# Performance work log

Measured on AMD Instinct MI355X. Metric: run time of the kernel, lower is better.

Reference implementation:

```python
import jax, jax.numpy as jnp
import numpy as np

K = 76          # model dim = 6 + 30 + 30 + 10 (concat of modality embeddings)
H = 8           # heads; per-head dim == K (wide attention variant)
D = 6           # depth
T = 1024        # seq_length (frames)
B = 8           # batch
C = 2           # num_classes
EPS = 1e-5


def setup_inputs() -> dict:
    key = jax.random.key(0)
    ks = jax.random.split(key, 24)
    rn = lambda k, shape, s=0.02: (jax.random.normal(k, shape, jnp.float32) * s)
    return {
        # forward inputs (per-frame multimodal features)
        "v": jax.random.normal(ks[0], (B, T, 6), jnp.float32),
        "x": jax.random.normal(ks[1], (B, T, 137), jnp.float32),
        "y": jax.random.normal(ks[2], (B, T, 113), jnp.float32),
        "z": jax.random.normal(ks[3], (B, T, 35), jnp.float32),
        # modality embed linears (stored (in, out); torch does x @ W.T)
        "W_hp": rn(ks[4], (6, 6)),     "b_hp": jnp.zeros((6,), jnp.float32),
        "W_lm": rn(ks[5], (137, 30)),  "b_lm": jnp.zeros((30,), jnp.float32),
        "W_el": rn(ks[6], (113, 30)),  "b_el": jnp.zeros((30,), jnp.float32),
        "W_au": rn(ks[7], (35, 10)),   "b_au": jnp.zeros((10,), jnp.float32),
        "pos_emb": rn(ks[8], (T, K)),
        # per-block params stacked over depth for lax.scan
        "Wq": rn(ks[9], (D, K, H * K)),
        "Wk": rn(ks[10], (D, K, H * K)),
        "Wv": rn(ks[11], (D, K, H * K)),
        "Wu": rn(ks[12], (D, H * K, K)), "bu": jnp.zeros((D, K), jnp.float32),
        "ln1_s": jnp.ones((D, K), jnp.float32), "ln1_b": jnp.zeros((D, K), jnp.float32),
        "W1": rn(ks[13], (D, K, 4 * K)), "b1": jnp.zeros((D, 4 * K), jnp.float32),
        "W2": rn(ks[14], (D, 4 * K, K)), "b2": jnp.zeros((D, K), jnp.float32),
        "ln2_s": jnp.ones((D, K), jnp.float32), "ln2_b": jnp.zeros((D, K), jnp.float32),
        "W_out": rn(ks[15], (K, C)), "b_out": jnp.zeros((C,), jnp.float32),
    }


def _layernorm(h, s, b):
    mu = jnp.mean(h, axis=-1, keepdims=True)
    var = jnp.mean(jnp.square(h - mu), axis=-1, keepdims=True)
    return (h - mu) * jax.lax.rsqrt(var + EPS) * s + b


def reference(v, x, y, z,
              W_hp, b_hp, W_lm, b_lm, W_el, b_el, W_au, b_au,
              pos_emb, Wq, Wk, Wv, Wu, bu, ln1_s, ln1_b,
              W1, b1, W2, b2, ln2_s, ln2_b, W_out, b_out):
    b, t = v.shape[0], v.shape[1]
    tokens = jnp.concatenate([
        v @ W_hp + b_hp,
        x @ W_lm + b_lm,
        y @ W_el + b_el,
        z @ W_au + b_au,
    ], axis=2)                                   # (b, t, K)
    h = tokens + pos_emb[None, :, :]
    scale = 1.0 / np.sqrt(K)                     # dot / sqrt(e), e == k

    def block(hh, p):
        wq, wk, wv, wu, bu_, l1s, l1b, w1, b1_, w2, b2_, l2s, l2b = p
        # (b, t, H*K) -> (b, H, t, K); per-head dim is full K here
        q = (hh @ wq).reshape(b, t, H, K).transpose(0, 2, 1, 3)
        k_ = (hh @ wk).reshape(b, t, H, K).transpose(0, 2, 1, 3)
        vv = (hh @ wv).reshape(b, t, H, K).transpose(0, 2, 1, 3)
        dot = jax.nn.softmax(jnp.einsum('bhte,bhse->bhts', q, k_) * scale, axis=-1)
        att = jnp.einsum('bhts,bhse->bhte', dot, vv)        # (b, H, t, K)
        att = att.transpose(0, 2, 1, 3).reshape(b, t, H * K)
        att = att @ wu + bu_                                # unify heads -> (b, t, K)
        h1 = _layernorm(att + hh, l1s, l1b)
        ff = jax.nn.relu(h1 @ w1 + b1_) @ w2 + b2_
        return _layernorm(ff + h1, l2s, l2b), None

    h, _ = jax.lax.scan(
        block, h,
        (Wq, Wk, Wv, Wu, bu, ln1_s, ln1_b, W1, b1, W2, b2, ln2_s, ln2_b))
    return h @ W_out + b_out                     # (b, t, num_classes)
```

## Files before the change

kernel.cpp:

```cpp
#include <hip/hip_runtime.h>
#include <hip/hip_bf16.h>
#include <math.h>

#define B_   8
#define T_   1024
#define K_   76
#define KP_  96
#define H_   8
#define D_   6
#define C_   2
#define HK_  608
#define QKLD_ 640
#define FF_  304
#define FFP_ 320
#define EK_  320
#define BT_  8192
#define EPS_ 1e-5f
#define SCL2_ (0.11470786693528088f * 1.4426950408889634f)

typedef unsigned short u16;
typedef unsigned int u32;
typedef short bf16x8 __attribute__((ext_vector_type(8)));
typedef float f32x4 __attribute__((ext_vector_type(4)));

__device__ __forceinline__ u16 f2b(float f) {
  __hip_bfloat16 h = __float2bfloat16(f);
  return *reinterpret_cast<u16*>(&h);
}
__device__ __forceinline__ float b2f(u16 u) {
  __hip_bfloat16 h = *reinterpret_cast<__hip_bfloat16*>(&u);
  return __bfloat162float(h);
}
__device__ __forceinline__ u32 pack2(float a, float b) {
  __hip_bfloat162 t = __float22bfloat162_rn(make_float2(a, b));
  return *reinterpret_cast<u32*>(&t);
}

#define PER_L_ 304128ULL
__global__ __launch_bounds__(256) void wconv_kernel(
    const float* __restrict__ Wq, const float* __restrict__ Wk, const float* __restrict__ Wv,
    const float* __restrict__ Wu, const float* __restrict__ W1, const float* __restrict__ W2,
    u16* __restrict__ WT) {
  __shared__ float Ls[32][65];
  int zz = blockIdx.y;
  int d = zz / 6, wt = zz % 6;
  const float* in; int Kd, Nsrc, Nalloc, Kp; u16* out;
  size_t lb = (size_t)d * PER_L_;
  switch (wt) {
    case 0: in = Wq + (size_t)d*K_*HK_; Kd=K_;  Nsrc=HK_; Nalloc=640; Kp=KP_;  out = WT + lb;          break;
    case 1: in = Wk + (size_t)d*K_*HK_; Kd=K_;  Nsrc=HK_; Nalloc=640; Kp=KP_;  out = WT + lb + 61440;  break;
    case 2: in = Wv + (size_t)d*K_*HK_; Kd=K_;  Nsrc=HK_; Nalloc=640; Kp=KP_;  out = WT + lb + 122880; break;
    case 3: in = Wu + (size_t)d*HK_*K_; Kd=HK_; Nsrc=K_;  Nalloc=96;  Kp=HK_;  out = WT + lb + 184320; break;
    case 4: in = W1 + (size_t)d*K_*FF_; Kd=K_;  Nsrc=FF_; Nalloc=320; Kp=KP_;  out = WT + lb + 242688; break;
    default:in = W2 + (size_t)d*FF_*K_; Kd=FF_; Nsrc=K_;  Nalloc=96;  Kp=FFP_; out = WT + lb + 273408; break;
  }
  int tiles_k = Kp / 32;
  int tiles_n = (Nalloc + 63) / 64;
  int tile = blockIdx.x;
  if (tile >= tiles_k * tiles_n) return;
  int tn = tile / tiles_k, tk = tile % tiles_k;
  int n0 = tn * 64, k0 = tk * 32;
  for (int i = threadIdx.x; i < 2048; i += 256) {
    int kk = i >> 6, nn = i & 63;
    int gk = k0 + kk, gn = n0 + nn;
    int srccol = gn;
    if (wt < 3) {
      int hh8 = gn / 80, ft = gn - hh8 * 80;
      srccol = (ft < 76) ? (hh8 * 76 + ft) : -1;
    }
    Ls[kk][nn] = (gk < Kd && srccol >= 0 && srccol < Nsrc) ? in[(size_t)gk * Nsrc + srccol] : 0.f;
  }
  __syncthreads();
  for (int i = threadIdx.x; i < 2048; i += 256) {
    int nn = i >> 5, kk = i & 31;
    int gn = n0 + nn;
    if (gn < Nalloc) out[(size_t)gn * Kp + k0 + kk] = f2b(Ls[kk][nn]);
  }
}

__global__ void wembed_kernel(const float* __restrict__ W_hp, const float* __restrict__ b_hp,
                              const float* __restrict__ W_lm, const float* __restrict__ b_lm,
                              const float* __restrict__ W_el, const float* __restrict__ b_el,
                              const float* __restrict__ W_au, const float* __restrict__ b_au,
                              u16* __restrict__ WE) {
  int idx = blockIdx.x * 256 + threadIdx.x;
  if (idx >= 96 * EK_) return;
  int n = idx / EK_, kk = idx % EK_;
  float val = 0.f;
  if (n < 76) {
    if (kk < 6) { if (n < 6) val = W_hp[kk * 6 + n]; }
    else if (kk < 143) { int i = kk - 6; if (n >= 6 && n < 36) val = W_lm[i * 30 + (n - 6)]; }
    else if (kk < 256) { int i = kk - 143; if (n >= 36 && n < 66) val = W_el[i * 30 + (n - 36)]; }
    else if (kk < 291) { int i = kk - 256; if (n >= 66) val = W_au[i * 10 + (n - 66)]; }
    else if (kk == 291) {
      val = (n < 6) ? b_hp[n] : (n < 36) ? b_lm[n - 6] : (n < 66) ? b_el[n - 36] : b_au[n - 66];
    }
  }
  WE[idx] = f2b(val);
}

__global__ void pack_kernel(const float* __restrict__ v, const float* __restrict__ x,
                            const float* __restrict__ y, const float* __restrict__ z,
                            u16* __restrict__ xin) {
  int idx = blockIdx.x * 256 + threadIdx.x;
  if (idx >= BT_ * (EK_ / 2)) return;
  int bt = idx / (EK_ / 2), dc = idx % (EK_ / 2);
  int c0 = dc * 2;
  auto fetch = [&](int c) -> float {
    if (c < 6) return v[bt * 6 + c];
    if (c < 143) return x[bt * 137 + c - 6];
    if (c < 256) return y[bt * 113 + c - 143];
    if (c < 291) return z[bt * 35 + c - 256];
    if (c == 291) return 1.0f;
    return 0.f;
  };
  ((u32*)xin)[idx] = pack2(fetch(c0), fetch(c0 + 1));
}

template<int RT, int CT, int KSTEPS, int RELU, int TPB>
__global__ __launch_bounds__(TPB) void gemm_kernel(
    const u16* __restrict__ A, int lda,
    const u16* __restrict__ Wt, int ldw, unsigned long long wstride,
    const float* __restrict__ bias,
    u16* __restrict__ Cc, int ldc, int N,
    int ksplit, int klen, unsigned long long osplit,
    float cs,
    u16* __restrict__ vbt,
    const float* __restrict__ pos) {
  __shared__ u16 Bs[CT * 16 * 56];
  const int tid = threadIdx.x;
  const int w = tid >> 6, lane = tid & 63;
  const int r = lane & 15, g = lane >> 4;
  const int n0 = blockIdx.x * CT * 16;
  const int m0 = blockIdx.y * (TPB / 64) * 16 * RT;
  const int z = blockIdx.z;
  const int k0 = z * ksplit;
  const int kend = k0 + klen;
  const u16* Wz = Wt + (size_t)z * wstride;
  const float* bias_eff = (z == 0) ? bias : nullptr;
  const float csz = (z == 0) ? cs : 1.f;
  u16* Cz = Cc + (size_t)z * osplit;
  constexpr int NB = (CT * 64 + TPB - 1) / TPB;

  const f32x4 fz = {0.f, 0.f, 0.f, 0.f};
  f32x4 acc[RT][CT];
  #pragma unroll
  for (int rt = 0; rt < RT; rt++)
    #pragma unroll
    for (int ct = 0; ct < CT; ct++) acc[rt][ct] = fz;

  bf16x8 a_all[RT][KSTEPS];
  #pragma unroll
  for (int rt = 0; rt < RT; rt++) {
    const u16* arow = A + (size_t)(m0 + (w * RT + rt) * 16 + r) * lda;
    #pragma unroll
    for (int ks = 0; ks < KSTEPS; ks++) {
      int kA = k0 + ks * 32 + g * 8;
      if (kA < kend) a_all[rt][ks] = *(const bf16x8*)(arow + kA);
      else a_all[rt][ks] = bf16x8{0, 0, 0, 0, 0, 0, 0, 0};
    }
  }

  uint4 bpre[NB];
  auto loadB = [&](int ks) {
    int kk = k0 + ks * 32;
    #pragma unroll
    for (int i0 = 0; i0 < NB; i0++) {
      int idx = tid + i0 * TPB;
      bpre[i0] = make_uint4(0, 0, 0, 0);
      if (idx < CT * 64) {
        int nn = idx >> 2, kc = idx & 3;
        if (kk + kc * 8 < kend)
          bpre[i0] = *(const uint4*)(Wz + (size_t)(n0 + nn) * ldw + kk + kc * 8);
      }
    }
  };
  loadB(0);

  for (int ks = 0; ks < KSTEPS; ks++) {
    __syncthreads();
    #pragma unroll
    for (int i0 = 0; i0 < NB; i0++) {
      int idx = tid + i0 * TPB;
      if (idx < CT * 64) {
        int nn = idx >> 2, kc = idx & 3;
        *(uint4*)&Bs[nn * 56 + (((kc ^ (nn & 3)) << 3))] = bpre[i0];
      }
    }
    __syncthreads();
    if (ks + 1 < KSTEPS) loadB(ks + 1);
    #pragma unroll
    for (int ct = 0; ct < CT; ct++) {
      bf16x8 bb = *(const bf16x8*)&Bs[(ct * 16 + r) * 56 + (((g ^ (r & 3)) << 3))];
      #pragma unroll
      for (int rt = 0; rt < RT; rt++)
        acc[rt][ct] = __builtin_amdgcn_mfma_f32_16x16x32_bf16(a_all[rt][ks], bb, acc[rt][ct], 0, 0, 0);
    }
  }

  if (vbt && z == 2) {
    #pragma unroll
    for (int rt = 0; rt < RT; rt++) {
      #pragma unroll
      for (int ct = 0; ct < CT; ct++) {
        int feat = ct * 16 + r;
        int token = m0 + (w * RT + rt) * 16 + g * 4;
        int bb_ = token >> 10, tt = token & 1023;
        ushort4 pk;
        if (feat < 76) {
          pk.x = f2b(acc[rt][ct][0]); pk.y = f2b(acc[rt][ct][1]);
          pk.z = f2b(acc[rt][ct][2]); pk.w = f2b(acc[rt][ct][3]);
        } else {
          pk = make_ushort4(0, 0, 0, 0);
        }
        *(ushort4*)(vbt + (((size_t)(bb_ * 8 + blockIdx.x) * 80 + feat) << 10) + tt) = pk;
      }
    }
  } else {
    #pragma unroll
    for (int rt = 0; rt < RT; rt++) {
      #pragma unroll
      for (int ct = 0; ct < CT; ct++) {
        int col = n0 + ct * 16 + r;
        if (col < ldc) {
          #pragma unroll
          for (int reg = 0; reg < 4; reg++) {
            int row = m0 + (w * RT + rt) * 16 + g * 4 + reg;
            float val = acc[rt][ct][reg] * csz;
            if (bias_eff && col < N) val += bias_eff[col];
            if (pos && col < N) val += pos[(row & (T_ - 1)) * K_ + col];
            if (RELU) val = fmaxf(val, 0.f);
            Cz[(size_t)row * ldc + col] = f2b(val);
          }
        }
      }
    }
  }
}

__global__ __launch_bounds__(64) void ffn_kernel(
    const u16* __restrict__ att, const u16* __restrict__ WuT, const float* __restrict__ bu,
    const u16* __restrict__ hres, const float* __restrict__ l1s, const float* __restrict__ l1b,
    const u16* __restrict__ W1T, const float* __restrict__ b1,
    const u16* __restrict__ W2T, const float* __restrict__ b2,
    const float* __restrict__ l2s, const float* __restrict__ l2b,
    u16* __restrict__ hout) {
  __shared__ u16 Bs[6 * 16 * 56];
  __shared__ u16 h1s[16 * 104];
  __shared__ u16 ffs[16 * 328];
  const int lane = threadIdx.x & 63;
  const int r = lane & 15, g = lane >> 4;
  const int m0 = blockIdx.x * 16;
  const f32x4 fz = {0.f, 0.f, 0.f, 0.f};

  u16 resv[4][6];
  #pragma unroll
  for (int reg = 0; reg < 4; reg++)
    #pragma unroll
    for (int ct = 0; ct < 6; ct++)
      resv[reg][ct] = hres[(size_t)(m0 + g * 4 + reg) * KP_ + ct * 16 + r];

  bf16x8 a1[19];
  {
    const u16* arow = att + (size_t)(m0 + r) * HK_;
    #pragma unroll
    for (int ks = 0; ks < 19; ks++) a1[ks] = *(const bf16x8*)(arow + ks * 32 + g * 8);
  }
  f32x4 acc1[6];
  #pragma unroll
  for (int ct = 0; ct < 6; ct++) acc1[ct] = fz;
  {
    uint4 bpre[6];
    auto loadB1 = [&](int ks) {
      #pragma unroll
      for (int i0 = 0; i0 < 6; i0++) {
        int idx = lane + i0 * 64;
        int nn = idx >> 2, kc = idx & 3;
        bpre[i0] = *(const uint4*)(WuT + (size_t)nn * HK_ + ks * 32 + kc * 8);
      }
    };
    loadB1(0);
    for (int ks = 0; ks < 19; ks++) {
      #pragma unroll
      for (int i0 = 0; i0 < 6; i0++) {
        int idx = lane + i0 * 64;
        int nn = idx >> 2, kc = idx & 3;
        *(uint4*)&Bs[nn * 56 + ((kc ^ (nn & 3)) << 3)] = bpre[i0];
      }
      if (ks + 1 < 19) loadB1(ks + 1);
      #pragma unroll
      for (int ct = 0; ct < 6; ct++) {
        bf16x8 bb = *(const bf16x8*)&Bs[(ct * 16 + r) * 56 + ((g ^ (r & 3)) << 3)];
        acc1[ct] = __builtin_amdgcn_mfma_f32_16x16x32_bf16(a1[ks], bb, acc1[ct], 0, 0, 0);
      }
    }
  }
  #pragma unroll
  for (int reg = 0; reg < 4; reg++) {
    float vals[6];
    float s = 0.f, s2 = 0.f;
    #pragma unroll
    for (int ct = 0; ct < 6; ct++) {
      int col = ct * 16 + r;
      float val = 0.f;
      if (col < K_) {
        val = acc1[ct][reg] + bu[col] + b2f(resv[reg][ct]);
        s += val; s2 += val * val;
      }
      vals[ct] = val;
    }
    #pragma unroll
    for (int m = 1; m < 16; m <<= 1) { s += __shfl_xor(s, m); s2 += __shfl_xor(s2, m); }
    float mu = s * (1.f / 76.f);
    float rstd = rsqrtf(s2 * (1.f / 76.f) - mu * mu + EPS_);
    #pragma unroll
    for (int ct = 0; ct < 6; ct++) {
      int col = ct * 16 + r;
      u16 ov = 0;
      if (col < K_) ov = f2b((vals[ct] - mu) * rstd * l1s[col] + l1b[col]);
      h1s[(g * 4 + reg) * 104 + col] = ov;
    }
  }

  bf16x8 a2[3];
  #pragma unroll
  for (int ks = 0; ks < 3; ks++)
    a2[ks] = *(const bf16x8*)&h1s[r * 104 + ks * 32 + g * 8];
  f32x4 acc2[20];
  #pragma unroll
  for (int ct = 0; ct < 20; ct++) acc2[ct] = fz;
  #pragma unroll
  for (int ks = 0; ks < 3; ks++) {
    bf16x8 bb[20];
    #pragma unroll
    for (int ct = 0; ct < 20; ct++)
      bb[ct] = *(const bf16x8*)(W1T + (size_t)(ct * 16 + r) * KP_ + ks * 32 + g * 8);
    #pragma unroll
    for (int ct = 0; ct < 20; ct++)
      acc2[ct] = __builtin_amdgcn_mfma_f32_16x16x32_bf16(a2[ks], bb[ct], acc2[ct], 0, 0, 0);
  }
  #pragma unroll
  for (int reg = 0; reg < 4; reg++)
    #pragma unroll
    for (int ct = 0; ct < 20; ct++) {
      int col = ct * 16 + r;
      float val = acc2[ct][reg] + ((col < FF_) ? b1[col] : 0.f);
      ffs[(g * 4 + reg) * 328 + col] = f2b(fmaxf(val, 0.f));
    }

  bf16x8 a3[10];
  #pragma unroll
  for (int ks = 0; ks < 10; ks++)
    a3[ks] = *(const bf16x8*)&ffs[r * 328 + ks * 32 + g * 8];
  f32x4 acc3[6];
  #pragma unroll
  for (int ct = 0; ct < 6; ct++) acc3[ct] = fz;
  {
    uint4 bpre[6];
    auto loadB3 = [&](int ks) {
      #pragma unroll
      for (int i0 = 0; i0 < 6; i0++) {
        int idx = lane + i0 * 64;
        int nn = idx >> 2, kc = idx & 3;
        bpre[i0] = *(const uint4*)(W2T + (size_t)nn * FFP_ + ks * 32 + kc * 8);
      }
    };
    loadB3(0);
    for (int ks = 0; ks < 10; ks++) {
      #pragma unroll
      for (int i0 = 0; i0 < 6; i0++) {
        int idx = lane + i0 * 64;
        int nn = idx >> 2, kc = idx & 3;
        *(uint4*)&Bs[nn * 56 + ((kc ^ (nn & 3)) << 3)] = bpre[i0];
      }
      if (ks + 1 < 10) loadB3(ks + 1);
      #pragma unroll
      for (int ct = 0; ct < 6; ct++) {
        bf16x8 bb = *(const bf16x8*)&Bs[(ct * 16 + r) * 56 + ((g ^ (r & 3)) << 3)];
        acc3[ct] = __builtin_amdgcn_mfma_f32_16x16x32_bf16(a3[ks], bb, acc3[ct], 0, 0, 0);
      }
    }
  }
  #pragma unroll
  for (int reg = 0; reg < 4; reg++) {
    float vals[6];
    float s = 0.f, s2 = 0.f;
    #pragma unroll
    for (int ct = 0; ct < 6; ct++) {
      int col = ct * 16 + r;
      float val = 0.f;
      if (col < K_) {
        val = acc3[ct][reg] + b2[col] + b2f(h1s[(g * 4 + reg) * 104 + col]);
        s += val; s2 += val * val;
      }
      vals[ct] = val;
    }
    #pragma unroll
    for (int m = 1; m < 16; m <<= 1) { s += __shfl_xor(s, m); s2 += __shfl_xor(s2, m); }
    float mu = s * (1.f / 76.f);
    float rstd = rsqrtf(s2 * (1.f / 76.f) - mu * mu + EPS_);
    u16* outr = hout + (size_t)(m0 + g * 4 + reg) * KP_;
    #pragma unroll
    for (int ct = 0; ct < 6; ct++) {
      int col = ct * 16 + r;
      u16 ov = 0;
      if (col < K_) ov = f2b((vals[ct] - mu) * rstd * l2s[col] + l2b[col]);
      outr[col] = ov;
    }
  }
}

__global__ __launch_bounds__(256, 3) void attn_kernel(const u16* __restrict__ q,
                                                      const u16* __restrict__ k,
                                                      const u16* __restrict__ vbt,
                                                      u16* __restrict__ att) {
  __shared__ u16 Ks[64 * 104];
  __shared__ u16 Vs[80 * 72];
  __shared__ u32 Psw[128 * 36];
  const int bid = blockIdx.x;
  const int hh = bid & 7, b = (bid >> 3) & 7, qt = bid >> 6;
  const int tid = threadIdx.x;
  const int w = tid >> 6, lane = tid & 63;
  const int r = lane & 15, g = lane >> 4;
  const int qbase = b * T_ + qt * 128;

  bf16x8 aq[2][3];
  #pragma unroll
  for (int rt = 0; rt < 2; rt++) {
    const u16* qsrc = q + (size_t)(qbase + w * 32 + rt * 16 + r) * QKLD_ + hh * 80;
    #pragma unroll
    for (int ks = 0; ks < 3; ks++) {
      int e0 = ks * 32 + g * 8;
      aq[rt][ks] = (e0 < 80) ? *(const bf16x8*)(qsrc + e0) : bf16x8{0, 0, 0, 0, 0, 0, 0, 0};
    }
  }

  const int krow = tid >> 2, kq4 = tid & 3;
  uint4 kpre[3], vpre[3];
  auto stage_load = [&](int kt) {
    const int kb = b * T_ + kt * 64;
    const u16* ksrc = k + (size_t)(kb + krow) * QKLD_ + hh * 80;
    #pragma unroll
    for (int i = 0; i < 3; i++) {
      int c = kq4 + 4 * i;
      kpre[i] = (c < 10) ? *(const uint4*)(ksrc + c * 8) : make_uint4(0, 0, 0, 0);
    }
    const u16* vsrc = vbt + (((size_t)(b * 8 + hh) * 80) << 10) + kt * 64;
    #pragma unroll
    for (int p = 0; p < 3; p++) {
      int idx = tid + p * 256;
      vpre[p] = (idx < 640) ? *(const uint4*)(vsrc + ((size_t)(idx >> 3) << 10) + (idx & 7) * 8)
                            : make_uint4(0, 0, 0, 0);
    }
  };
  auto stage_write = [&]() {
    #pragma unroll
    for (int i = 0; i < 3; i++) {
      int c = kq4 + 4 * i;
      *(uint4*)&Ks[krow * 104 + c * 8] = kpre[i];
    }
    #pragma unroll
    for (int p = 0; p < 3; p++) {
      int idx = tid + p * 256;
      if (idx < 640)
        *(uint4*)&Vs[(idx >> 3) * 72 + (idx & 7) * 8] = vpre[p];
    }
  };

  u32* Pw = Psw + w * 32 * 36;

  const f32x4 fz = {0.f, 0.f, 0.f, 0.f};
  f32x4 o[2][5];
  float ls[2] = {0.f, 0.f};
  #pragma unroll
  for (int rt = 0; rt < 2; rt++)
    #pragma unroll
    for (int i = 0; i < 5; i++) o[rt][i] = fz;

  stage_load(0);

  for (int kt = 0; kt < 16; kt++) {
    __syncthreads();
    stage_write();
    __syncthreads();
    if (kt < 15) stage_load(kt + 1);

    f32x4 st[2][4];
    #pragma unroll
    for (int ct = 0; ct < 4; ct++) { st[0][ct] = fz; st[1][ct] = fz; }
    __builtin_amdgcn_s_setprio(1);
    #pragma unroll
    for (int ct = 0; ct < 4; ct++) {
      #pragma unroll
      for (int ks = 0; ks < 3; ks++) {
        bf16x8 ak = *(const bf16x8*)&Ks[(ct * 16 + r) * 104 + ks * 32 + g * 8];
        st[0][ct] = __builtin_amdgcn_mfma_f32_16x16x32_bf16(ak, aq[0][ks], st[0][ct], 0, 0, 0);
        st[1][ct] = __builtin_amdgcn_mfma_f32_16x16x32_bf16(ak, aq[1][ks], st[1][ct], 0, 0, 0);
      }
    }
    __builtin_amdgcn_s_setprio(0);

    #pragma unroll
    for (int rt = 0; rt < 2; rt++) {
      float rs = 0.f;
      u32 pk[8];
      #pragma unroll
      for (int ct = 0; ct < 4; ct++) {
        float p0 = exp2f(st[rt][ct][0]), p1 = exp2f(st[rt][ct][1]);
        float p2 = exp2f(st[rt][ct][2]), p3 = exp2f(st[rt][ct][3]);
        rs += (p0 + p1) + (p2 + p3);
        pk[ct * 2] = pack2(p0, p1);
        pk[ct * 2 + 1] = pack2(p2, p3);
      }
      ls[rt] += rs;
      u32* pw = Pw + (rt * 16 + r) * 36;
      #pragma unroll
      for (int ct = 0; ct < 4; ct++)
        *(uint2*)(pw + ct * 8 + g * 2) = make_uint2(pk[ct * 2], pk[ct * 2 + 1]);
    }

    bf16x8 pa[2][2];
    #pragma unroll
    for (int rt = 0; rt < 2; rt++) {
      const u32* pr = Pw + (rt * 16 + r) * 36;
      #pragma unroll
      for (int ks = 0; ks < 2; ks++) {
        uint4 t = *(const uint4*)(pr + ks * 16 + g * 4);
        pa[rt][ks] = *reinterpret_cast<bf16x8*>(&t);
      }
    }
    __builtin_amdgcn_s_setprio(1);
    #pragma unroll
    for (int ks = 0; ks < 2; ks++) {
      #pragma unroll
      for (int c5 = 0; c5 < 5; c5++) {
        bf16x8 av = *(const bf16x8*)&Vs[(c5 * 16 + r) * 72 + ks * 32 + g * 8];
        #pragma unroll
        for (int rt = 0; rt < 2; rt++)
          o[rt][c5] = __builtin_amdgcn_mfma_f32_16x16x32_bf16(av, pa[rt][ks], o[rt][c5], 0, 0, 0);
      }
    }
    __builtin_amdgcn_s_setprio(0);
  }

  #pragma unroll
  for (int rt = 0; rt < 2; rt++) {
    ls[rt] += __shfl_xor(ls[rt], 16);
    ls[rt] += __shfl_xor(ls[rt], 32);
    float inv = 1.f / ls[rt];
    int token = qbase + w * 32 + rt * 16 + r;
    #pragma unroll
    for (int c5 = 0; c5 < 5; c5++) {
      if (c5 == 4 && g == 3) continue;
      ushort4 pk4;
      pk4.x = f2b(o[rt][c5][0] * inv);
      pk4.y = f2b(o[rt][c5][1] * inv);
      pk4.z = f2b(o[rt][c5][2] * inv);
      pk4.w = f2b(o[rt][c5][3] * inv);
      *(ushort4*)&att[(size_t)token * HK_ + hh * 76 + c5 * 16 + g * 4] = pk4;
    }
  }
}

__global__ void out_kernel(const u16* __restrict__ h, const float* __restrict__ W,
                           const float* __restrict__ bias, float* __restrict__ out) {
  int bt = blockIdx.x * 256 + threadIdx.x;
  if (bt >= BT_) return;
  const u32* hr = (const u32*)(h + (size_t)bt * KP_);
  float acc0 = bias[0], acc1 = bias[1];
  #pragma unroll 4
  for (int d = 0; d < 38; d++) {
    u32 h2 = hr[d];
    float f0 = b2f((u16)(h2 & 0xffff)), f1 = b2f((u16)(h2 >> 16));
    acc0 += f0 * W[(2 * d) * 2] + f1 * W[(2 * d + 1) * 2];
    acc1 += f0 * W[(2 * d) * 2 + 1] + f1 * W[(2 * d + 1) * 2 + 1];
  }
  out[bt * 2] = acc0;
  out[bt * 2 + 1] = acc1;
}

extern "C" void kernel_launch(void* const* d_in, const int* in_sizes, int n_in,
                              void* d_out, int out_size, void* d_ws, size_t ws_size,
                              hipStream_t stream) {
  const float* v    = (const float*)d_in[0];
  const float* x    = (const float*)d_in[1];
  const float* y    = (const float*)d_in[2];
  const float* z    = (const float*)d_in[3];
  const float* W_hp = (const float*)d_in[4];
  const float* b_hp = (const float*)d_in[5];
  const float* W_lm = (const float*)d_in[6];
  const float* b_lm = (const float*)d_in[7];
  const float* W_el = (const float*)d_in[8];
  const float* b_el = (const float*)d_in[9];
  const float* W_au = (const float*)d_in[10];
  const float* b_au = (const float*)d_in[11];
  const float* pos  = (const float*)d_in[12];
  const float* Wq   = (const float*)d_in[13];
  const float* Wk   = (const float*)d_in[14];
  const float* Wv   = (const float*)d_in[15];
  const float* Wu   = (const float*)d_in[16];
  const float* bu   = (const float*)d_in[17];
  const float* ln1s = (const float*)d_in[18];
  const float* ln1b = (const float*)d_in[19];
  const float* W1   = (const float*)d_in[20];
  const float* b1   = (const float*)d_in[21];
  const float* W2   = (const float*)d_in[22];
  const float* b2   = (const float*)d_in[23];
  const float* ln2s = (const float*)d_in[24];
  const float* ln2b = (const float*)d_in[25];
  const float* Wout = (const float*)d_in[26];
  const float* bout = (const float*)d_in[27];

  u16* ws  = (u16*)d_ws;
  u16* WT  = ws;
  u16* WE  = WT + 1824768;
  u16* h   = WE + 30720;
  u16* xin = h + 786432;
  u16* qb  = xin + 2621440;
  u16* kb  = qb + 5242880;
  u16* vbt = kb + 5242880;
  u16* att = vbt + 5242880;
  u16* h1  = att + 4980736;

  wconv_kernel<<<dim3(38, 36), 256, 0, stream>>>(Wq, Wk, Wv, Wu, W1, W2, WT);
  wembed_kernel<<<(96 * EK_ + 255) / 256, 256, 0, stream>>>(
      W_hp, b_hp, W_lm, b_lm, W_el, b_el, W_au, b_au, WE);
  pack_kernel<<<(BT_ * (EK_ / 2) + 255) / 256, 256, 0, stream>>>(v, x, y, z, xin);
  gemm_kernel<1, 6, 10, 0, 128><<<dim3(1, 256, 1), 128, 0, stream>>>(
      xin, EK_, WE, EK_, 0ULL, nullptr, h, KP_, K_, 0, EK_, 0ULL,
      1.f, nullptr, pos);

  for (int d = 0; d < D_; d++) {
    u16* WTd = WT + (size_t)d * PER_L_;
    const float* bu_d = bu + (size_t)d * K_;
    const float* l1s  = ln1s + (size_t)d * K_;
    const float* l1b  = ln1b + (size_t)d * K_;
    const float* b1_d = b1 + (size_t)d * FF_;
    const float* b2_d = b2 + (size_t)d * K_;
    const float* l2s  = ln2s + (size_t)d * K_;
    const float* l2b  = ln2b + (size_t)d * K_;

    gemm_kernel<2, 5, 3, 0, 256><<<dim3(8, 64, 3), 256, 0, stream>>>(
        h, KP_, WTd, KP_, 61440ULL, nullptr, qb, QKLD_, QKLD_, 0, KP_, 5242880ULL,
        SCL2_, vbt, nullptr);
    attn_kernel<<<dim3(512), 256, 0, stream>>>(qb, kb, vbt, att);
    ffn_kernel<<<dim3(512), 64, 0, stream>>>(
        att, WTd + 184320, bu_d, h, l1s, l1b,
        WTd + 242688, b1_d, WTd + 273408, b2_d, l2s, l2b, h);
  }

  out_kernel<<<(BT_ + 255) / 256, 256, 0, stream>>>(h, Wout, bout, (float*)d_out);
}
```

Before: 571.3 us.

## Merge prep kernels, fuse output head into FFN, halve attention tile size

Folds the three preprocessing launches into one prep kernel that dispatches on block index. Moves the final output projection into the last layer's FFN epilogue using a shuffle reduction, which removes a separate launch and a reread of h. It also changes attention from 128-query tiles with 256 threads to 64-query tiles with 128 threads over 1024 blocks, using different K/V staging and zeroed pad columns. This trades fewer launches and better occupancy against reloading each K/V tile for twice as many blocks.

```diff
diff --git a/kernel.cpp b/kernel.cpp
--- a/kernel.cpp
+++ b/kernel.cpp
@@ -37,84 +37,84 @@
 }
 
 #define PER_L_ 304128ULL
-__global__ __launch_bounds__(256) void wconv_kernel(
+__global__ __launch_bounds__(256) void prep_kernel(
     const float* __restrict__ Wq, const float* __restrict__ Wk, const float* __restrict__ Wv,
     const float* __restrict__ Wu, const float* __restrict__ W1, const float* __restrict__ W2,
-    u16* __restrict__ WT) {
+    u16* __restrict__ WT,
+    const float* __restrict__ W_hp, const float* __restrict__ b_hp,
+    const float* __restrict__ W_lm, const float* __restrict__ b_lm,
+    const float* __restrict__ W_el, const float* __restrict__ b_el,
+    const float* __restrict__ W_au, const float* __restrict__ b_au,
+    u16* __restrict__ WE,
+    const float* __restrict__ v, const float* __restrict__ x,
+    const float* __restrict__ y, const float* __restrict__ z,
+    u16* __restrict__ xin) {
   __shared__ float Ls[32][65];
-  int zz = blockIdx.y;
-  int d = zz / 6, wt = zz % 6;
-  const float* in; int Kd, Nsrc, Nalloc, Kp; u16* out;
-  size_t lb = (size_t)d * PER_L_;
-  switch (wt) {
-    case 0: in = Wq + (size_t)d*K_*HK_; Kd=K_;  Nsrc=HK_; Nalloc=640; Kp=KP_;  out = WT + lb;          break;
-    case 1: in = Wk + (size_t)d*K_*HK_; Kd=K_;  Nsrc=HK_; Nalloc=640; Kp=KP_;  out = WT + lb + 61440;  break;
-    case 2: in = Wv + (size_t)d*K_*HK_; Kd=K_;  Nsrc=HK_; Nalloc=640; Kp=KP_;  out = WT + lb + 122880; break;
-    case 3: in = Wu + (size_t)d*HK_*K_; Kd=HK_; Nsrc=K_;  Nalloc=96;  Kp=HK_;  out = WT + lb + 184320; break;
-    case 4: in = W1 + (size_t)d*K_*FF_; Kd=K_;  Nsrc=FF_; Nalloc=320; Kp=KP_;  out = WT + lb + 242688; break;
-    default:in = W2 + (size_t)d*FF_*K_; Kd=FF_; Nsrc=K_;  Nalloc=96;  Kp=FFP_; out = WT + lb + 273408; break;
-  }
-  int tiles_k = Kp / 32;
-  int tiles_n = (Nalloc + 63) / 64;
-  int tile = blockIdx.x;
-  if (tile >= tiles_k * tiles_n) return;
-  int tn = tile / tiles_k, tk = tile % tiles_k;
-  int n0 = tn * 64, k0 = tk * 32;
-  for (int i = threadIdx.x; i < 2048; i += 256) {
-    int kk = i >> 6, nn = i & 63;
-    int gk = k0 + kk, gn = n0 + nn;
-    int srccol = gn;
-    if (wt < 3) {
-      int hh8 = gn / 80, ft = gn - hh8 * 80;
-      srccol = (ft < 76) ? (hh8 * 76 + ft) : -1;
-    }
-    Ls[kk][nn] = (gk < Kd && srccol >= 0 && srccol < Nsrc) ? in[(size_t)gk * Nsrc + srccol] : 0.f;
-  }
-  __syncthreads();
-  for (int i = threadIdx.x; i < 2048; i += 256) {
-    int nn = i >> 5, kk = i & 31;
-    int gn = n0 + nn;
-    if (gn < Nalloc) out[(size_t)gn * Kp + k0 + kk] = f2b(Ls[kk][nn]);
-  }
-}
-
-__global__ void wembed_kernel(const float* __restrict__ W_hp, const float* __restrict__ b_hp,
-                              const float* __restrict__ W_lm, const float* __restrict__ b_lm,
-                              const float* __restrict__ W_el, const float* __restrict__ b_el,
-                              const float* __restrict__ W_au, const float* __restrict__ b_au,
-                              u16* __restrict__ WE) {
-  int idx = blockIdx.x * 256 + threadIdx.x;
-  if (idx >= 96 * EK_) return;
-  int n = idx / EK_, kk = idx % EK_;
-  float val = 0.f;
-  if (n < 76) {
-    if (kk < 6) { if (n < 6) val = W_hp[kk * 6 + n]; }
-    else if (kk < 143) { int i = kk - 6; if (n >= 6 && n < 36) val = W_lm[i * 30 + (n - 6)]; }
-    else if (kk < 256) { int i = kk - 143; if (n >= 36 && n < 66) val = W_el[i * 30 + (n - 36)]; }
-    else if (kk < 291) { int i = kk - 256; if (n >= 66) val = W_au[i * 10 + (n - 66)]; }
-    else if (kk == 291) {
-      val = (n < 6) ? b_hp[n] : (n < 36) ? b_lm[n - 6] : (n < 66) ? b_el[n - 36] : b_au[n - 66];
-    }
-  }
-  WE[idx] = f2b(val);
-}
-
-__global__ void pack_kernel(const float* __restrict__ v, const float* __restrict__ x,
-                            const float* __restrict__ y, const float* __restrict__ z,
-                            u16* __restrict__ xin) {
-  int idx = blockIdx.x * 256 + threadIdx.x;
-  if (idx >= BT_ * (EK_ / 2)) return;
-  int bt = idx / (EK_ / 2), dc = idx % (EK_ / 2);
-  int c0 = dc * 2;
-  auto fetch = [&](int c) -> float {
-    if (c < 6) return v[bt * 6 + c];
-    if (c < 143) return x[bt * 137 + c - 6];
-    if (c < 256) return y[bt * 113 + c - 143];
-    if (c < 291) return z[bt * 35 + c - 256];
-    if (c == 291) return 1.0f;
-    return 0.f;
-  };
-  ((u32*)xin)[idx] = pack2(fetch(c0), fetch(c0 + 1));
+  const int bid = blockIdx.x;
+  if (bid < 1368) {
+    int tile = bid % 38, zz = bid / 38;
+    int d = zz / 6, wt = zz % 6;
+    const float* in; int Kd, Nsrc, Nalloc, Kp; u16* out;
+    size_t lb = (size_t)d * PER_L_;
+    switch (wt) {
+      case 0: in = Wq + (size_t)d*K_*HK_; Kd=K_;  Nsrc=HK_; Nalloc=640; Kp=KP_;  out = WT + lb;          break;
+      case 1: in = Wk + (size_t)d*K_*HK_; Kd=K_;  Nsrc=HK_; Nalloc=640; Kp=KP_;  out = WT + lb + 61440;  break;
+      case 2: in = Wv + (size_t)d*K_*HK_; Kd=K_;  Nsrc=HK_; Nalloc=640; Kp=KP_;  out = WT + lb + 122880; break;
+      case 3: in = Wu + (size_t)d*HK_*K_; Kd=HK_; Nsrc=K_;  Nalloc=96;  Kp=HK_;  out = WT + lb + 184320; break;
+      case 4: in = W1 + (size_t)d*K_*FF_; Kd=K_;  Nsrc=FF_; Nalloc=320; Kp=KP_;  out = WT + lb + 242688; break;
+      default:in = W2 + (size_t)d*FF_*K_; Kd=FF_; Nsrc=K_;  Nalloc=96;  Kp=FFP_; out = WT + lb + 273408; break;
+    }
+    int tiles_k = Kp / 32;
+    int tiles_n = (Nalloc + 63) / 64;
+    if (tile >= tiles_k * tiles_n) return;
+    int tn = tile / tiles_k, tk = tile % tiles_k;
+    int n0 = tn * 64, k0 = tk * 32;
+    for (int i = threadIdx.x; i < 2048; i += 256) {
+      int kk = i >> 6, nn = i & 63;
+      int gk = k0 + kk, gn = n0 + nn;
+      int srccol = gn;
+      if (wt < 3) {
+        int hh8 = gn / 80, ft = gn - hh8 * 80;
+        srccol = (ft < 76) ? (hh8 * 76 + ft) : -1;
+      }
+      Ls[kk][nn] = (gk < Kd && srccol >= 0 && srccol < Nsrc) ? in[(size_t)gk * Nsrc + srccol] : 0.f;
+    }
+    __syncthreads();
+    for (int i = threadIdx.x; i < 2048; i += 256) {
+      int nn = i >> 5, kk = i & 31;
+      int gn = n0 + nn;
+      if (gn < Nalloc) out[(size_t)gn * Kp + k0 + kk] = f2b(Ls[kk][nn]);
+    }
+  } else if (bid < 1488) {
+    int idx = (bid - 1368) * 256 + threadIdx.x;
+    if (idx >= 96 * EK_) return;
+    int n = idx / EK_, kk = idx % EK_;
+    float val = 0.f;
+    if (n < 76) {
+      if (kk < 6) { if (n < 6) val = W_hp[kk * 6 + n]; }
+      else if (kk < 143) { int i = kk - 6; if (n >= 6 && n < 36) val = W_lm[i * 30 + (n - 6)]; }
+      else if (kk < 256) { int i = kk - 143; if (n >= 36 && n < 66) val = W_el[i * 30 + (n - 36)]; }
+      else if (kk < 291) { int i = kk - 256; if (n >= 66) val = W_au[i * 10 + (n - 66)]; }
+      else if (kk == 291) {
+        val = (n < 6) ? b_hp[n] : (n < 36) ? b_lm[n - 6] : (n < 66) ? b_el[n - 36] : b_au[n - 66];
+      }
+    }
+    WE[idx] = f2b(val);
+  } else {
+    int idx = (bid - 1488) * 256 + threadIdx.x;
+    if (idx >= BT_ * (EK_ / 2)) return;
+    int bt = idx / (EK_ / 2), dc = idx % (EK_ / 2);
+    int c0 = dc * 2;
+    auto fetch = [&](int c) -> float {
+      if (c < 6) return v[bt * 6 + c];
+      if (c < 143) return x[bt * 137 + c - 6];
+      if (c < 256) return y[bt * 113 + c - 143];
+      if (c < 291) return z[bt * 35 + c - 256];
+      if (c == 291) return 1.0f;
+      return 0.f;
+    };
+    ((u32*)xin)[idx] = pack2(fetch(c0), fetch(c0 + 1));
+  }
 }
 
 template<int RT, int CT, int KSTEPS, int RELU, int TPB>
@@ -244,7 +244,9 @@
     const u16* __restrict__ W1T, const float* __restrict__ b1,
     const u16* __restrict__ W2T, const float* __restrict__ b2,
     const float* __restrict__ l2s, const float* __restrict__ l2b,
-    u16* __restrict__ hout) {
+    u16* __restrict__ hout,
+    const float* __restrict__ Wout, const float* __restrict__ bout,
+    float* __restrict__ outp) {
   __shared__ u16 Bs[6 * 16 * 56];
   __shared__ u16 h1s[16 * 104];
   __shared__ u16 ffs[16 * 328];
@@ -400,29 +402,51 @@
     float mu = s * (1.f / 76.f);
     float rstd = rsqrtf(s2 * (1.f / 76.f) - mu * mu + EPS_);
     u16* outr = hout + (size_t)(m0 + g * 4 + reg) * KP_;
+    float p0 = 0.f, p1 = 0.f;
     #pragma unroll
     for (int ct = 0; ct < 6; ct++) {
       int col = ct * 16 + r;
       u16 ov = 0;
-      if (col < K_) ov = f2b((vals[ct] - mu) * rstd * l2s[col] + l2b[col]);
+      if (col < K_) {
+        float vln = (vals[ct] - mu) * rstd * l2s[col] + l2b[col];
+        ov = f2b(vln);
+        if (outp) {
+          p0 += vln * Wout[col * 2];
+          p1 += vln * Wout[col * 2 + 1];
+        }
+      }
       outr[col] = ov;
     }
-  }
-}
-
-__global__ __launch_bounds__(256, 3) void attn_kernel(const u16* __restrict__ q,
+    if (outp) {
+      #pragma unroll
+      for (int m = 1; m < 16; m <<= 1) { p0 += __shfl_xor(p0, m); p1 += __shfl_xor(p1, m); }
+      if (r == 0) {
+        int row = m0 + g * 4 + reg;
+        outp[row * 2] = p0 + bout[0];
+        outp[row * 2 + 1] = p1 + bout[1];
+      }
+    }
+  }
+}
+
+__global__ __launch_bounds__(128, 2) void attn_kernel(const u16* __restrict__ q,
                                                       const u16* __restrict__ k,
                                                       const u16* __restrict__ vbt,
                                                       u16* __restrict__ att) {
   __shared__ u16 Ks[64 * 104];
   __shared__ u16 Vs[80 * 72];
-  __shared__ u32 Psw[128 * 36];
+  __shared__ u32 Psw[64 * 36];
   const int bid = blockIdx.x;
   const int hh = bid & 7, b = (bid >> 3) & 7, qt = bid >> 6;
   const int tid = threadIdx.x;
   const int w = tid >> 6, lane = tid & 63;
   const int r = lane & 15, g = lane >> 4;
-  const int qbase = b * T_ + qt * 128;
+  const int qbase = b * T_ + qt * 64;
+
+  {
+    int row = tid >> 1, off = 80 + (tid & 1) * 8;
+    *(uint4*)&Ks[row * 104 + off] = make_uint4(0, 0, 0, 0);
+  }
 
   bf16x8 aq[2][3];
   #pragma unroll
@@ -435,35 +459,29 @@
     }
   }
 
-  const int krow = tid >> 2, kq4 = tid & 3;
-  uint4 kpre[3], vpre[3];
+  const int krow = tid >> 1, kq2 = tid & 1;
+  uint4 kpre[5], vpre[5];
   auto stage_load = [&](int kt) {
     const int kb = b * T_ + kt * 64;
     const u16* ksrc = k + (size_t)(kb + krow) * QKLD_ + hh * 80;
     #pragma unroll
-    for (int i = 0; i < 3; i++) {
-      int c = kq4 + 4 * i;
-      kpre[i] = (c < 10) ? *(const uint4*)(ksrc + c * 8) : make_uint4(0, 0, 0, 0);
-    }
+    for (int i = 0; i < 5; i++)
+      kpre[i] = *(const uint4*)(ksrc + (kq2 + 2 * i) * 8);
     const u16* vsrc = vbt + (((size_t)(b * 8 + hh) * 80) << 10) + kt * 64;
     #pragma unroll
-    for (int p = 0; p < 3; p++) {
-      int idx = tid + p * 256;
-      vpre[p] = (idx < 640) ? *(const uint4*)(vsrc + ((size_t)(idx >> 3) << 10) + (idx & 7) * 8)
-                            : make_uint4(0, 0, 0, 0);
+    for (int p = 0; p < 5; p++) {
+      int idx = tid + p * 128;
+      vpre[p] = *(const uint4*)(vsrc + ((size_t)(idx >> 3) << 10) + (idx & 7) * 8);
     }
   };
   auto stage_write = [&]() {
     #pragma unroll
-    for (int i = 0; i < 3; i++) {
-      int c = kq4 + 4 * i;
-      *(uint4*)&Ks[krow * 104 + c * 8] = kpre[i];
-    }
-    #pragma unroll
-    for (int p = 0; p < 3; p++) {
-      int idx = tid + p * 256;
-      if (idx < 640)
-        *(uint4*)&Vs[(idx >> 3) * 72 + (idx & 7) * 8] = vpre[p];
+    for (int i = 0; i < 5; i++)
+      *(uint4*)&Ks[krow * 104 + (kq2 + 2 * i) * 8] = kpre[i];
+    #pragma unroll
+    for (int p = 0; p < 5; p++) {
+      int idx = tid + p * 128;
+      *(uint4*)&Vs[(idx >> 3) * 72 + (idx & 7) * 8] = vpre[p];
     }
   };
 
@@ -560,23 +578,6 @@
       *(ushort4*)&att[(size_t)token * HK_ + hh * 76 + c5 * 16 + g * 4] = pk4;
     }
   }
-}
-
-__global__ void out_kernel(const u16* __restrict__ h, const float* __restrict__ W,
-                           const float* __restrict__ bias, float* __restrict__ out) {
-  int bt = blockIdx.x * 256 + threadIdx.x;
-  if (bt >= BT_) return;
-  const u32* hr = (const u32*)(h + (size_t)bt * KP_);
-  float acc0 = bias[0], acc1 = bias[1];
-  #pragma unroll 4
-  for (int d = 0; d < 38; d++) {
-    u32 h2 = hr[d];
-    float f0 = b2f((u16)(h2 & 0xffff)), f1 = b2f((u16)(h2 >> 16));
-    acc0 += f0 * W[(2 * d) * 2] + f1 * W[(2 * d + 1) * 2];
-    acc1 += f0 * W[(2 * d) * 2 + 1] + f1 * W[(2 * d + 1) * 2 + 1];
-  }
-  out[bt * 2] = acc0;
-  out[bt * 2 + 1] = acc1;
 }
 
 extern "C" void kernel_launch(void* const* d_in, const int* in_sizes, int n_in,
@@ -620,12 +621,11 @@
   u16* kb  = qb + 5242880;
   u16* vbt = kb + 5242880;
   u16* att = vbt + 5242880;
-  u16* h1  = att + 4980736;
-
-  wconv_kernel<<<dim3(38, 36), 256, 0, stream>>>(Wq, Wk, Wv, Wu, W1, W2, WT);
-  wembed_kernel<<<(96 * EK_ + 255) / 256, 256, 0, stream>>>(
-      W_hp, b_hp, W_lm, b_lm, W_el, b_el, W_au, b_au, WE);
-  pack_kernel<<<(BT_ * (EK_ / 2) + 255) / 256, 256, 0, stream>>>(v, x, y, z, xin);
+
+  prep_kernel<<<dim3(6608), 256, 0, stream>>>(
+      Wq, Wk, Wv, Wu, W1, W2, WT,
+      W_hp, b_hp, W_lm, b_lm, W_el, b_el, W_au, b_au, WE,
+      v, x, y, z, xin);
   gemm_kernel<1, 6, 10, 0, 128><<<dim3(1, 256, 1), 128, 0, stream>>>(
       xin, EK_, WE, EK_, 0ULL, nullptr, h, KP_, K_, 0, EK_, 0ULL,
       1.f, nullptr, pos);
@@ -643,11 +643,10 @@
     gemm_kernel<2, 5, 3, 0, 256><<<dim3(8, 64, 3), 256, 0, stream>>>(
         h, KP_, WTd, KP_, 61440ULL, nullptr, qb, QKLD_, QKLD_, 0, KP_, 5242880ULL,
         SCL2_, vbt, nullptr);
-    attn_kernel<<<dim3(512), 256, 0, stream>>>(qb, kb, vbt, att);
+    attn_kernel<<<dim3(1024), 128, 0, stream>>>(qb, kb, vbt, att);
     ffn_kernel<<<dim3(512), 64, 0, stream>>>(
         att, WTd + 184320, bu_d, h, l1s, l1b,
-        WTd + 242688, b1_d, WTd + 273408, b2_d, l2s, l2b, h);
-  }
-
-  out_kernel<<<(BT_ + 255) / 256, 256, 0, stream>>>(h, Wout, bout, (float*)d_out);
-}
+        WTd + 242688, b1_d, WTd + 273408, b2_d, l2s, l2b, h,
+        Wout, bout, (d == D_ - 1) ? (float*)d_out : nullptr);
+  }
+}
```

Measured after the change: 871.9 us. 52.6% more time.
